# Performance work log

Measured on AMD Instinct MI355X. Metric: run time of the kernel, lower is better.

Reference implementation:

```python
import jax, jax.numpy as jnp
import numpy as np

B, F0, D = 2048, 39, 16
LAYER_SIZES = [128, 128, 128]  # split_half=True -> field_nums [39, 64, 64]


def setup_inputs() -> dict:
    key = jax.random.key(0)
    ks = jax.random.split(key, 1 + 2 * len(LAYER_SIZES))
    inputs = jax.random.normal(ks[0], (B, F0, D), dtype=jnp.float32)
    out = {"inputs": inputs}
    field_nums = [F0]
    for i, size in enumerate(LAYER_SIZES):
        fk = field_nums[-1]
        fan_in = F0 * fk  # conv1d filter fan-in (kernel width 1)
        scale = np.sqrt(2.0 / (fan_in + size)).astype(np.float32)  # glorot
        # filter stored as [F0, Fk, size]; TF flat index is h0*Fk + hk
        out[f"w{i}"] = jax.random.normal(ks[1 + 2 * i], (F0, fk, size), dtype=jnp.float32) * scale
        out[f"b{i}"] = jnp.zeros((size,), dtype=jnp.float32)
        field_nums.append(size // 2)  # split_half=True
    return out


def reference(inputs, w0, w1, w2, b0, b1, b2):
    # CIN: per-embedding-dim outer product of x0 and x_{k-1}, then 1x1 conv
    # (shared dense over field pairs). Fused here as a single einsum per layer.
    x0 = inputs  # [B, F0, D]
    xk = inputs  # [B, Fk, D]
    params = [(w0, b0), (w1, b1), (w2, b2)]
    n_layers = len(params)
    direct = []
    for idx, (W, b) in enumerate(params):
        # out[b, s, d] = sum_{h,k} x0[b,h,d] * xk[b,k,d] * W[h,k,s]
        z = jnp.einsum('bhd,bkd,hks->bsd', x0, xk, W) + b[None, :, None]
        z = jax.nn.relu(z)  # activation='relu'
        if idx != n_layers - 1:
            half = z.shape[1] // 2  # split_half: first half feeds next layer
            xk = z[:, :half, :]
            direct.append(z[:, half:, :])
        else:
            direct.append(z)
    logit = jnp.sum(jnp.concatenate(direct, axis=1), axis=-1)  # [B, 64+64+128]
    return logit
```

## Files before the change

### kernel.cpp

```cpp
#include <hip/hip_runtime.h>
#include <stdint.h>
#include <stddef.h>

#define F0N  39
#define SN   128
#define NB   4
#define X0TS 45
#define XKTS 72
#define WBLK 8192
#define NHB2 234

typedef __attribute__((ext_vector_type(8))) short short8;
typedef __attribute__((ext_vector_type(4))) float floatx4;

__device__ __forceinline__ uint16_t f2bf(float f) {
  uint32_t u = __float_as_uint(f);
  u += 0x7fffu + ((u >> 16) & 1u);
  return (uint16_t)(u >> 16);
}

__global__ __launch_bounds__(256) void cin_prepass(
    const float* __restrict__ w0, const float* __restrict__ w1,
    const float* __restrict__ w2, uint16_t* __restrict__ wt) {
  __shared__ float T[32 * 132];
  const int bc = blockIdx.x;
  const int ch = bc & 1;
  const int lh = bc >> 1;
  const int L = lh / F0N;
  const int h = lh - L * F0N;
  const float* W = (L == 0) ? w0 : ((L == 1) ? w1 : w2);
  const int fk = (L == 0) ? 39 : 64;
  const int tid = threadIdx.x;

  for (int e = tid; e < 4096; e += 256) {
    int kc = e >> 7, s = e & 127;
    int k = ch * 32 + kc;
    T[kc * 132 + s] = (k < fk) ? W[(h * fk + k) * SN + s] : 0.0f;
  }
  __syncthreads();
  uint32_t* dst = (uint32_t*)(wt + (size_t)lh * WBLK);
  for (int i = tid; i < 2048; i += 256) {
    int st = i >> 8, w = i & 255;
    int ln = w >> 2, jp = w & 3;
    int quad = ln >> 4, l16 = ln & 15;
    int k0 = quad * 8 + jp * 2;
    int s = st * 16 + l16;
    dst[(size_t)(st * 2 + ch) * 256 + w] =
        (uint32_t)f2bf(T[k0 * 132 + s]) | ((uint32_t)f2bf(T[(k0 + 1) * 132 + s]) << 16);
  }
}

__global__ __launch_bounds__(1024, 4) void cin_main(
    const float* __restrict__ x,
    const float* __restrict__ bias0, const float* __restrict__ bias1,
    const float* __restrict__ bias2,
    const uint16_t* __restrict__ wt,
    float* __restrict__ out) {

  __shared__ __align__(16) float    X0T[NB * 16 * X0TS];
  __shared__ __align__(16) uint16_t XKT[NB * 16 * XKTS];

  const int tid  = threadIdx.x;
  const int lane = tid & 63;
  const int wave = tid >> 6;
  const int st   = wave >> 1;
  const int bg   = wave & 1;
  const int l16  = lane & 15;
  const int quad = lane >> 4;
  const int bbase = blockIdx.x * NB;

  {
    float* p = X0T;
#pragma unroll
    for (int i = 0; i < 3; i++) { int e = tid + 1024 * i; if (e < NB * 16 * X0TS) p[e] = 0.f; }
    uint32_t* q = (uint32_t*)XKT;
#pragma unroll
    for (int i = 0; i < 3; i++) { int e = tid + 1024 * i; if (e < NB * 16 * XKTS / 2) q[e] = 0u; }
  }
  __syncthreads();

#pragma unroll
  for (int it = 0; it < 3; ++it) {
    int e = tid + it * 1024;
    if (e < NB * F0N * 16) {
      float v = x[(size_t)bbase * (F0N * 16) + e];
      int d = e & 15, p = e >> 4;
      int b = p / F0N, h = p - b * F0N;
      X0T[(b * 16 + d) * X0TS + h] = v;
    }
  }
  __syncthreads();

  if (tid < 64 * NB) {
    int b = tid >> 6, d = (tid >> 2) & 15, kg = tid & 3;
    const float* src = &X0T[(b * 16 + d) * X0TS];
    uint32_t* drow = (uint32_t*)&XKT[(b * 16 + d) * XKTS + kg * 16];
#pragma unroll
    for (int i2 = 0; i2 < 8; i2++) {
      int k0 = kg * 16 + i2 * 2;
      uint32_t lo = (k0 < 39)     ? (uint32_t)f2bf(src[k0])     : 0u;
      uint32_t hi = (k0 + 1 < 39) ? (uint32_t)f2bf(src[k0 + 1]) : 0u;
      drow[i2] = lo | (hi << 16);
    }
  }
  __syncthreads();

  const int stlane = st * 1024 + lane * 8;

  short8 Wc0 = *(const short8*)(wt + stlane);
  short8 Wc1 = *(const short8*)(wt + stlane + 512);

  int ih = 0;
#pragma unroll 1
  for (int L = 0; L < 3; ++L) {
    short8 Bf0[2], Bf1[2];
#pragma unroll
    for (int bi = 0; bi < 2; ++bi) {
      const uint16_t* r = XKT + ((bg * 2 + bi) * 16 + l16) * XKTS + quad * 8;
      Bf0[bi] = *(const short8*)r;
      Bf1[bi] = *(const short8*)(r + 32);
    }
    const float* bp = (L == 0) ? bias0 : ((L == 1) ? bias1 : bias2);
    float bvr[4];
#pragma unroll
    for (int r = 0; r < 4; ++r) bvr[r] = bp[st * 16 + quad * 4 + r];

    floatx4 z[2] = {};
    const floatx4 zero4 = {0.f, 0.f, 0.f, 0.f};

#pragma unroll 1
    for (int h = 0; h < 39; ++h, ++ih) {
      int ihn = ih + 1;
      if (ihn > 116) ihn = 116;
      const uint16_t* wb = wt + (size_t)ihn * WBLK + stlane;
      short8 Wn0 = *(const short8*)(wb);
      short8 Wn1 = *(const short8*)(wb + 512);

      float xs[2];
#pragma unroll
      for (int bi = 0; bi < 2; ++bi)
        xs[bi] = X0T[((bg * 2 + bi) * 16 + l16) * X0TS + h];

#pragma unroll
      for (int bi = 0; bi < 2; ++bi) {
        floatx4 y = __builtin_amdgcn_mfma_f32_16x16x32_bf16(Wc0, Bf0[bi], zero4, 0, 0, 0);
        y = __builtin_amdgcn_mfma_f32_16x16x32_bf16(Wc1, Bf1[bi], y, 0, 0, 0);
#pragma unroll
        for (int r = 0; r < 4; ++r) z[bi][r] += xs[bi] * y[r];
      }
      Wc0 = Wn0;
      Wc1 = Wn1;
    }

#pragma unroll
    for (int bi = 0; bi < 2; ++bi) {
      const int b = bg * 2 + bi;
#pragma unroll
      for (int r = 0; r < 4; ++r) {
        float t = fmaxf(z[bi][r] + bvr[r], 0.f);
        if (L < 2 && st < 4)
          XKT[(b * 16 + l16) * XKTS + st * 16 + quad * 4 + r] = f2bf(t);
        float s4 = t;
        s4 += __shfl_xor(s4, 1);
        s4 += __shfl_xor(s4, 2);
        s4 += __shfl_xor(s4, 4);
        s4 += __shfl_xor(s4, 8);
        if (l16 == 0) {
          int s = st * 16 + quad * 4 + r;
          if (L == 2)       out[(size_t)(bbase + b) * 256 + 128 + s] = s4;
          else if (s >= 64) out[(size_t)(bbase + b) * 256 + L * 64 + (s - 64)] = s4;
        }
      }
    }
    if (L < 2) __syncthreads();
  }
}

extern "C" void kernel_launch(void* const* d_in, const int* in_sizes, int n_in,
                              void* d_out, int out_size, void* d_ws, size_t ws_size,
                              hipStream_t stream) {
  (void)in_sizes; (void)n_in; (void)out_size; (void)ws_size;
  const float* x  = (const float*)d_in[0];
  const float* w0 = (const float*)d_in[1];
  const float* b0 = (const float*)d_in[2];
  const float* w1 = (const float*)d_in[3];
  const float* b1 = (const float*)d_in[4];
  const float* w2 = (const float*)d_in[5];
  const float* b2 = (const float*)d_in[6];
  uint16_t* wt    = (uint16_t*)d_ws;

  cin_prepass<<<NHB2, 256, 0, stream>>>(w0, w1, w2, wt);
  cin_main<<<2048 / NB, 1024, 0, stream>>>(x, b0, b1, b2, wt, (float*)d_out);
}
```

Before: 151.8 us.

## Fold x0 scaling into MFMA operand and accumulate directly in MFMA

Instead of running a per-h MFMA and then scaling its output by x0 on the VALU, each h step now forms the operand x0[h]*xk in fp32, packs it to bf16 with v_cvt_pk_bf16_f32, and accumulates straight into the MFMA accumulators. The batch tile grows from 4 to 8 per block, and each wave now covers two s-tiles and two batches, so every weight fragment feeds more MFMAs. The xk buffer is kept in fp32, the launch-bounds occupancy hint is dropped, and the separate bf16 conversion pass is removed. In exchange, the per-h product is rounded to bf16, which changes numerics, there is more VALU packing work per step, and register pressure may rise.

```diff
diff --git a/kernel.cpp b/kernel.cpp
--- a/kernel.cpp
+++ b/kernel.cpp
@@ -4,19 +4,26 @@
 
 #define F0N  39
 #define SN   128
-#define NB   4
+#define NB   8
 #define X0TS 45
-#define XKTS 72
+#define KS   76
 #define WBLK 8192
 #define NHB2 234
 
 typedef __attribute__((ext_vector_type(8))) short short8;
 typedef __attribute__((ext_vector_type(4))) float floatx4;
+typedef __attribute__((ext_vector_type(4))) uint32_t uint32x4;
 
 __device__ __forceinline__ uint16_t f2bf(float f) {
   uint32_t u = __float_as_uint(f);
   u += 0x7fffu + ((u >> 16) & 1u);
   return (uint16_t)(u >> 16);
+}
+
+__device__ __forceinline__ uint32_t cvtpk(float lo, float hi) {
+  uint32_t r;
+  asm("v_cvt_pk_bf16_f32 %0, %1, %2" : "=v"(r) : "v"(lo), "v"(hi));
+  return r;
 }
 
 __global__ __launch_bounds__(256) void cin_prepass(
@@ -50,128 +57,153 @@
   }
 }
 
-__global__ __launch_bounds__(1024, 4) void cin_main(
+__global__ __launch_bounds__(1024) void cin_main(
     const float* __restrict__ x,
     const float* __restrict__ bias0, const float* __restrict__ bias1,
     const float* __restrict__ bias2,
     const uint16_t* __restrict__ wt,
     float* __restrict__ out) {
 
-  __shared__ __align__(16) float    X0T[NB * 16 * X0TS];
-  __shared__ __align__(16) uint16_t XKT[NB * 16 * XKTS];
+  __shared__ __align__(16) float X0T[NB * 16 * X0TS];
+  __shared__ __align__(16) float XKF[NB * 16 * KS];
 
   const int tid  = threadIdx.x;
   const int lane = tid & 63;
   const int wave = tid >> 6;
-  const int st   = wave >> 1;
-  const int bg   = wave & 1;
+  const int stg  = wave >> 2;
+  const int bg   = wave & 3;
   const int l16  = lane & 15;
   const int quad = lane >> 4;
   const int bbase = blockIdx.x * NB;
 
   {
-    float* p = X0T;
 #pragma unroll
-    for (int i = 0; i < 3; i++) { int e = tid + 1024 * i; if (e < NB * 16 * X0TS) p[e] = 0.f; }
-    uint32_t* q = (uint32_t*)XKT;
+    for (int i = 0; i < 6; i++) { int e = tid + 1024 * i; if (e < NB * 16 * X0TS) X0T[e] = 0.f; }
 #pragma unroll
-    for (int i = 0; i < 3; i++) { int e = tid + 1024 * i; if (e < NB * 16 * XKTS / 2) q[e] = 0u; }
+    for (int i = 0; i < 10; i++) { int e = tid + 1024 * i; if (e < NB * 16 * KS) XKF[e] = 0.f; }
   }
   __syncthreads();
 
 #pragma unroll
-  for (int it = 0; it < 3; ++it) {
+  for (int it = 0; it < 5; ++it) {
     int e = tid + it * 1024;
     if (e < NB * F0N * 16) {
       float v = x[(size_t)bbase * (F0N * 16) + e];
       int d = e & 15, p = e >> 4;
-      int b = p / F0N, h = p - b * F0N;
-      X0T[(b * 16 + d) * X0TS + h] = v;
+      int bb = p / F0N, h = p - bb * F0N;
+      X0T[(bb * 16 + d) * X0TS + h] = v;
+      XKF[(bb * 16 + d) * KS + h] = v;
     }
   }
   __syncthreads();
 
-  if (tid < 64 * NB) {
-    int b = tid >> 6, d = (tid >> 2) & 15, kg = tid & 3;
-    const float* src = &X0T[(b * 16 + d) * X0TS];
-    uint32_t* drow = (uint32_t*)&XKT[(b * 16 + d) * XKTS + kg * 16];
-#pragma unroll
-    for (int i2 = 0; i2 < 8; i2++) {
-      int k0 = kg * 16 + i2 * 2;
-      uint32_t lo = (k0 < 39)     ? (uint32_t)f2bf(src[k0])     : 0u;
-      uint32_t hi = (k0 + 1 < 39) ? (uint32_t)f2bf(src[k0 + 1]) : 0u;
-      drow[i2] = lo | (hi << 16);
-    }
-  }
-  __syncthreads();
-
-  const int stlane = st * 1024 + lane * 8;
-
-  short8 Wc0 = *(const short8*)(wt + stlane);
-  short8 Wc1 = *(const short8*)(wt + stlane + 512);
+  const int row0 = (bg * 2 + 0) * 16 + l16;
+  const int row1 = (bg * 2 + 1) * 16 + l16;
+  const float* x0p0 = X0T + row0 * X0TS;
+  const float* x0p1 = X0T + row1 * X0TS;
+
+  const uint16_t* wbase = wt + stg * 2048 + (size_t)lane * 8;
+
+  short8 Wc0 = *(const short8*)(wbase);
+  short8 Wc1 = *(const short8*)(wbase + 512);
+  short8 Wc2 = *(const short8*)(wbase + 1024);
+  short8 Wc3 = *(const short8*)(wbase + 1536);
 
   int ih = 0;
 #pragma unroll 1
   for (int L = 0; L < 3; ++L) {
-    short8 Bf0[2], Bf1[2];
-#pragma unroll
-    for (int bi = 0; bi < 2; ++bi) {
-      const uint16_t* r = XKT + ((bg * 2 + bi) * 16 + l16) * XKTS + quad * 8;
-      Bf0[bi] = *(const short8*)r;
-      Bf1[bi] = *(const short8*)(r + 32);
-    }
-    const float* bp = (L == 0) ? bias0 : ((L == 1) ? bias1 : bias2);
-    float bvr[4];
-#pragma unroll
-    for (int r = 0; r < 4; ++r) bvr[r] = bp[st * 16 + quad * 4 + r];
-
-    floatx4 z[2] = {};
-    const floatx4 zero4 = {0.f, 0.f, 0.f, 0.f};
+    const float* xq0 = XKF + row0 * KS + quad * 8;
+    const float* xq1 = XKF + row1 * KS + quad * 8;
+    floatx4 ka0 = *(const floatx4*)(xq0);
+    floatx4 ka1 = *(const floatx4*)(xq0 + 4);
+    floatx4 ka2 = *(const floatx4*)(xq0 + 32);
+    floatx4 ka3 = *(const floatx4*)(xq0 + 36);
+    floatx4 kb0 = *(const floatx4*)(xq1);
+    floatx4 kb1 = *(const floatx4*)(xq1 + 4);
+    floatx4 kb2 = *(const floatx4*)(xq1 + 32);
+    floatx4 kb3 = *(const floatx4*)(xq1 + 36);
+    __syncthreads();
+
+    floatx4 acc0 = {0.f, 0.f, 0.f, 0.f};
+    floatx4 acc1 = {0.f, 0.f, 0.f, 0.f};
+    floatx4 acc2 = {0.f, 0.f, 0.f, 0.f};
+    floatx4 acc3 = {0.f, 0.f, 0.f, 0.f};
+
+    float xs0 = x0p0[0];
+    float xs1 = x0p1[0];
 
 #pragma unroll 1
     for (int h = 0; h < 39; ++h, ++ih) {
       int ihn = ih + 1;
       if (ihn > 116) ihn = 116;
-      const uint16_t* wb = wt + (size_t)ihn * WBLK + stlane;
-      short8 Wn0 = *(const short8*)(wb);
-      short8 Wn1 = *(const short8*)(wb + 512);
-
-      float xs[2];
-#pragma unroll
-      for (int bi = 0; bi < 2; ++bi)
-        xs[bi] = X0T[((bg * 2 + bi) * 16 + l16) * X0TS + h];
-
-#pragma unroll
-      for (int bi = 0; bi < 2; ++bi) {
-        floatx4 y = __builtin_amdgcn_mfma_f32_16x16x32_bf16(Wc0, Bf0[bi], zero4, 0, 0, 0);
-        y = __builtin_amdgcn_mfma_f32_16x16x32_bf16(Wc1, Bf1[bi], y, 0, 0, 0);
-#pragma unroll
-        for (int r = 0; r < 4; ++r) z[bi][r] += xs[bi] * y[r];
-      }
-      Wc0 = Wn0;
-      Wc1 = Wn1;
+      const uint16_t* wbn = wbase + (size_t)ihn * WBLK;
+      short8 Wn0 = *(const short8*)(wbn);
+      short8 Wn1 = *(const short8*)(wbn + 512);
+      short8 Wn2 = *(const short8*)(wbn + 1024);
+      short8 Wn3 = *(const short8*)(wbn + 1536);
+      float xsn0 = x0p0[h + 1];
+      float xsn1 = x0p1[h + 1];
+
+      floatx4 s0v = {xs0, xs0, xs0, xs0};
+      floatx4 s1v = {xs1, xs1, xs1, xs1};
+      floatx4 p0 = ka0 * s0v, p1 = ka1 * s0v, p2 = ka2 * s0v, p3 = ka3 * s0v;
+      uint32x4 ga0, ga1;
+      ga0[0] = cvtpk(p0[0], p0[1]); ga0[1] = cvtpk(p0[2], p0[3]);
+      ga0[2] = cvtpk(p1[0], p1[1]); ga0[3] = cvtpk(p1[2], p1[3]);
+      ga1[0] = cvtpk(p2[0], p2[1]); ga1[1] = cvtpk(p2[2], p2[3]);
+      ga1[2] = cvtpk(p3[0], p3[1]); ga1[3] = cvtpk(p3[2], p3[3]);
+      p0 = kb0 * s1v; p1 = kb1 * s1v; p2 = kb2 * s1v; p3 = kb3 * s1v;
+      uint32x4 gb0, gb1;
+      gb0[0] = cvtpk(p0[0], p0[1]); gb0[1] = cvtpk(p0[2], p0[3]);
+      gb0[2] = cvtpk(p1[0], p1[1]); gb0[3] = cvtpk(p1[2], p1[3]);
+      gb1[0] = cvtpk(p2[0], p2[1]); gb1[1] = cvtpk(p2[2], p2[3]);
+      gb1[2] = cvtpk(p3[0], p3[1]); gb1[3] = cvtpk(p3[2], p3[3]);
+      short8 GA0 = __builtin_bit_cast(short8, ga0);
+      short8 GA1 = __builtin_bit_cast(short8, ga1);
+      short8 GB0 = __builtin_bit_cast(short8, gb0);
+      short8 GB1 = __builtin_bit_cast(short8, gb1);
+
+      acc0 = __builtin_amdgcn_mfma_f32_16x16x32_bf16(Wc0, GA0, acc0, 0, 0, 0);
+      acc1 = __builtin_amdgcn_mfma_f32_16x16x32_bf16(Wc0, GB0, acc1, 0, 0, 0);
+      acc2 = __builtin_amdgcn_mfma_f32_16x16x32_bf16(Wc2, GA0, acc2, 0, 0, 0);
+      acc3 = __builtin_amdgcn_mfma_f32_16x16x32_bf16(Wc2, GB0, acc3, 0, 0, 0);
+      acc0 = __builtin_amdgcn_mfma_f32_16x16x32_bf16(Wc1, GA1, acc0, 0, 0, 0);
+      acc1 = __builtin_amdgcn_mfma_f32_16x16x32_bf16(Wc1, GB1, acc1, 0, 0, 0);
+      acc2 = __builtin_amdgcn_mfma_f32_16x16x32_bf16(Wc3, GA1, acc2, 0, 0, 0);
+      acc3 = __builtin_amdgcn_mfma_f32_16x16x32_bf16(Wc3, GB1, acc3, 0, 0, 0);
+
+      Wc0 = Wn0; Wc1 = Wn1; Wc2 = Wn2; Wc3 = Wn3;
+      xs0 = xsn0; xs1 = xsn1;
     }
 
-#pragma unroll
-    for (int bi = 0; bi < 2; ++bi) {
-      const int b = bg * 2 + bi;
-#pragma unroll
-      for (int r = 0; r < 4; ++r) {
-        float t = fmaxf(z[bi][r] + bvr[r], 0.f);
-        if (L < 2 && st < 4)
-          XKT[(b * 16 + l16) * XKTS + st * 16 + quad * 4 + r] = f2bf(t);
-        float s4 = t;
-        s4 += __shfl_xor(s4, 1);
-        s4 += __shfl_xor(s4, 2);
-        s4 += __shfl_xor(s4, 4);
-        s4 += __shfl_xor(s4, 8);
-        if (l16 == 0) {
-          int s = st * 16 + quad * 4 + r;
-          if (L == 2)       out[(size_t)(bbase + b) * 256 + 128 + s] = s4;
-          else if (s >= 64) out[(size_t)(bbase + b) * 256 + L * 64 + (s - 64)] = s4;
-        }
-      }
+    const float* bp = (L == 0) ? bias0 : ((L == 1) ? bias1 : bias2);
+#define EPI(ACC, STI, BI)                                                     \
+    {                                                                         \
+      const int b_ = bg * 2 + (BI);                                           \
+      const int s0 = (stg * 2 + (STI)) * 16 + quad * 4;                       \
+      _Pragma("unroll")                                                       \
+      for (int r = 0; r < 4; ++r) {                                           \
+        float t = fmaxf((ACC)[r] + bp[s0 + r], 0.f);                          \
+        if (L < 2 && stg < 2)                 \
+          XKF[(b_ * 16 + l16) * KS + s0 + r] = t;                             \
+        float s4 = t;                                \
+        s4 += __shfl_xor(s4, 1);                                              \
+        s4 += __shfl_xor(s4, 2);                                              \
+        s4 += __shfl_xor(s4, 4);                                              \
+        s4 += __shfl_xor(s4, 8);                                              \
+        if (l16 == 0) {                                                       \
+          int s = s0 + r;                                                     \
+          if (L == 2)       out[(size_t)(bbase + b_) * 256 + 128 + s] = s4;   \
+          else if (s >= 64) out[(size_t)(bbase + b_) * 256 + L * 64 + (s - 64)] = s4; \
+        }                                                                     \
+      }                                                                       \
     }
+    EPI(acc0, 0, 0)
+    EPI(acc1, 0, 1)
+    EPI(acc2, 1, 0)
+    EPI(acc3, 1, 1)
+#undef EPI
+
     if (L < 2) __syncthreads();
   }
 }
```

Result: slower. 160.1 us (+5.4%).
